# Kernel optimization log

Measured on AMD Instinct MI355X. Metric: run time of the kernel, lower is better.

## Reference

```python
import jax, jax.numpy as jnp
import numpy as np

N = 20000
E = 320000
IN_FEAT = 256
HID = 256
OUT_FEAT = 128


def setup_inputs() -> dict:
    key = jax.random.key(0)
    ks = jax.random.split(key, 10)
    inp = {
        "x": jax.random.normal(ks[0], (N, IN_FEAT), dtype=jnp.float32),
        "edge_src": jax.random.randint(ks[1], (E,), 0, N, dtype=jnp.int32),
        "edge_dst": jax.random.randint(ks[2], (E,), 0, N, dtype=jnp.int32),
        "edge_w": jax.random.uniform(ks[3], (E,), dtype=jnp.float32),
        # params (Linear weights stored as [out, in], torch convention)
        "W_emb": jax.random.normal(ks[4], (HID, IN_FEAT), dtype=jnp.float32) / np.sqrt(IN_FEAT),
        "W_gc1": jax.random.normal(ks[5], (HID, 2 * HID), dtype=jnp.float32) / np.sqrt(2 * HID),
        "b_gc1": jnp.zeros((HID,), dtype=jnp.float32),
        "W_gc2": jax.random.normal(ks[6], (HID, 2 * HID), dtype=jnp.float32) / np.sqrt(2 * HID),
        "b_gc2": jnp.zeros((HID,), dtype=jnp.float32),
        "W_fc": jax.random.normal(ks[7], (OUT_FEAT, HID), dtype=jnp.float32) / np.sqrt(HID),
    }
    return inp


def reference(x, edge_src, edge_dst, edge_w, W_emb, W_gc1, b_gc1, W_gc2, b_gc2, W_fc):
    n = x.shape[0]

    def adj_mul(h):
        msgs = h[edge_src] * edge_w[:, None]           # [E, hid]
        return jax.ops.segment_sum(msgs, edge_dst, num_segments=n)

    def gconv(h, W, b):
        cat = jnp.concatenate([h, adj_mul(h)], axis=1)  # [N, 2*hid]
        return cat @ W.T + b

    h = x @ W_emb.T                                    # embedding (no bias)
    h = h + jax.nn.relu(gconv(h, W_gc1, b_gc1))        # residual (dropout = eval identity)
    h = h + jax.nn.relu(gconv(h, W_gc2, b_gc2))
    out = h @ W_fc.T                                   # fc_last (no bias)
    out = out / jnp.sqrt(jnp.sum(out * out, axis=1, keepdims=True))
    return out
```

## Files before the change

kernel.cpp:

```cpp
#include <hip/hip_runtime.h>
#include <math.h>

#define N_NODES 20000
#define E_EDGES 320000
#define HID 256
#define OUT_FEAT 128
#define MPAD 20224
#define CAP 64

#define BM 128
#define BN 128
#define BK 64
#define LSTR 72

typedef __attribute__((ext_vector_type(8))) __bf16 bf16x8;
typedef __attribute__((ext_vector_type(4))) float floatx4;


#define WBLK 176
#define EBLK 1250

__global__ void convert_scatter_kernel(
    const float* __restrict__ w0, const float* __restrict__ w1,
    const float* __restrict__ w2, const float* __restrict__ w3,
    __bf16* __restrict__ o0, __bf16* __restrict__ o1,
    __bf16* __restrict__ o2, __bf16* __restrict__ o3,
    const int* __restrict__ src, const int* __restrict__ dst,
    const float* __restrict__ w, int* __restrict__ counts,
    int2* __restrict__ edges) {
    const int b = blockIdx.x;
    if (b < WBLK) {
        const size_t gi = ((size_t)b * 256 + threadIdx.x) * 8;
        const size_t s0 = 65536, s1 = s0 + 131072, s2 = s1 + 131072, s3 = s2 + 32768;
        if (gi >= s3) return;
        const float* srcp; __bf16* dstp; size_t off;
        if (gi < s0)      { srcp = w0; dstp = o0; off = gi; }
        else if (gi < s1) { srcp = w1; dstp = o1; off = gi - s0; }
        else if (gi < s2) { srcp = w2; dstp = o2; off = gi - s1; }
        else              { srcp = w3; dstp = o3; off = gi - s2; }
        float4 v0 = *(const float4*)(srcp + off);
        float4 v1 = *(const float4*)(srcp + off + 4);
        bf16x8 o;
        o[0] = (__bf16)v0.x; o[1] = (__bf16)v0.y; o[2] = (__bf16)v0.z; o[3] = (__bf16)v0.w;
        o[4] = (__bf16)v1.x; o[5] = (__bf16)v1.y; o[6] = (__bf16)v1.z; o[7] = (__bf16)v1.w;
        *(bf16x8*)(dstp + off) = o;
    } else {
        int e = (b - WBLK) * 256 + threadIdx.x;
        if (e < E_EDGES) {
            int d = dst[e];
            int p = atomicAdd(&counts[d], 1);
            edges[(size_t)d * CAP + p] = make_int2(src[e], __float_as_int(w[e]));
        }
    }
}


__global__ __launch_bounds__(256) void aggregate_kernel(
    const __bf16* __restrict__ h, const int* __restrict__ counts,
    const int2* __restrict__ edges, __bf16* __restrict__ agg) {
    const int w = threadIdx.x >> 6, lane = threadIdx.x & 63;
    const int half = lane >> 5, lh = lane & 31;
    const int d = blockIdx.x * 8 + w * 2 + half;
    const size_t base = (size_t)d * CAP;
    const int iters = (counts[d] + 15) >> 4;
    float acc[8];
#pragma unroll
    for (int q = 0; q < 8; q++) acc[q] = 0.f;

    for (int it = 0; it < iters; ++it) {
        const int2* ep = edges + base + it * 16;
        int4 eh[8];
#pragma unroll
        for (int u = 0; u < 8; u++) eh[u] = *(const int4*)(ep + u * 2);
        bf16x8 hv[16];
#pragma unroll
        for (int u = 0; u < 8; u++) {
            hv[u * 2]     = *(const bf16x8*)(h + (size_t)eh[u].x * HID + lh * 8);
            hv[u * 2 + 1] = *(const bf16x8*)(h + (size_t)eh[u].z * HID + lh * 8);
        }
#pragma unroll
        for (int u = 0; u < 8; u++) {
            float wa = __int_as_float(eh[u].y), wb = __int_as_float(eh[u].w);
#pragma unroll
            for (int q = 0; q < 8; q++) {
                acc[q] = fmaf(wa, (float)hv[u * 2][q], acc[q]);
                acc[q] = fmaf(wb, (float)hv[u * 2 + 1][q], acc[q]);
            }
        }
    }
    bf16x8 o;
#pragma unroll
    for (int q = 0; q < 8; q++) o[q] = (__bf16)acc[q];
    *(bf16x8*)(agg + (size_t)d * HID + lh * 8) = o;
}


template <int KTOT, int EPI, bool F32A>
__global__ __launch_bounds__(256) void gemm_tile_kernel(
    const __bf16* __restrict__ A1,
    const float* __restrict__ A1f,
    const __bf16* __restrict__ A2,
    const __bf16* __restrict__ W,
    const float* __restrict__ bias,
    const __bf16* __restrict__ hres,
    __bf16* __restrict__ outb)
{
    __shared__ __bf16 As[BM * LSTR];
    __shared__ __bf16 Bs[BN * LSTR];
    const int tid = threadIdx.x;
    const int row0 = blockIdx.y * BM;
    const int col0 = blockIdx.x * BN;
    const int wv = tid >> 6, l = tid & 63, lr = l & 15, lq = l >> 4;
    const int wm = wv & 1, wn = wv >> 1;

    floatx4 acc[4][4];
#pragma unroll
    for (int i = 0; i < 4; i++)
#pragma unroll
        for (int j = 0; j < 4; j++) acc[i][j] = (floatx4){0.f, 0.f, 0.f, 0.f};

    const int srow = tid >> 3;
    const int skq = (tid & 7) * 8;

    for (int kc = 0; kc < KTOT; kc += BK) {
        if (F32A) {
#pragma unroll
            for (int r = 0; r < 4; r++) {
                int row = r * 32 + srow;
                int grow = row0 + row;
                float4 v0 = make_float4(0.f, 0.f, 0.f, 0.f), v1 = v0;
                if (grow < N_NODES) {
                    const float* xp = A1f + (size_t)grow * HID + kc + skq;
                    v0 = *(const float4*)xp;
                    v1 = *(const float4*)(xp + 4);
                }
                bf16x8 o;
                o[0] = (__bf16)v0.x; o[1] = (__bf16)v0.y; o[2] = (__bf16)v0.z; o[3] = (__bf16)v0.w;
                o[4] = (__bf16)v1.x; o[5] = (__bf16)v1.y; o[6] = (__bf16)v1.z; o[7] = (__bf16)v1.w;
                *(bf16x8*)&As[row * LSTR + skq] = o;
            }
        } else {
            const __bf16* Asrc = (KTOT == 512 && kc >= 256) ? A2 : A1;
            const int ks = (KTOT == 512) ? (kc & 255) : kc;
#pragma unroll
            for (int r = 0; r < 4; r++) {
                int row = r * 32 + srow;
                *(bf16x8*)&As[row * LSTR + skq] =
                    *(const bf16x8*)(Asrc + (size_t)(row0 + row) * HID + ks + skq);
            }
        }
#pragma unroll
        for (int r = 0; r < 4; r++) {
            int row = r * 32 + srow;
            *(bf16x8*)&Bs[row * LSTR + skq] =
                *(const bf16x8*)(W + (size_t)(col0 + row) * KTOT + kc + skq);
        }
        __syncthreads();
#pragma unroll
        for (int s = 0; s < 2; s++) {
            bf16x8 af[4], bfr[4];
#pragma unroll
            for (int mt = 0; mt < 4; mt++)
                af[mt] = *(const bf16x8*)&As[(wm * 64 + mt * 16 + lr) * LSTR + s * 32 + lq * 8];
#pragma unroll
            for (int nt = 0; nt < 4; nt++)
                bfr[nt] = *(const bf16x8*)&Bs[(wn * 64 + nt * 16 + lr) * LSTR + s * 32 + lq * 8];
#pragma unroll
            for (int mt = 0; mt < 4; mt++)
#pragma unroll
                for (int nt = 0; nt < 4; nt++)
                    acc[mt][nt] = __builtin_amdgcn_mfma_f32_16x16x32_bf16(af[mt], bfr[nt], acc[mt][nt], 0, 0, 0);
        }
        __syncthreads();
    }

#pragma unroll
    for (int nt = 0; nt < 4; nt++) {
        const int col = col0 + wn * 64 + nt * 16 + lr;
        float b = 0.f;
        if (EPI == 1) b = bias[col];
#pragma unroll
        for (int mt = 0; mt < 4; mt++) {
            const int row = row0 + wm * 64 + mt * 16 + lq * 4;
#pragma unroll
            for (int r = 0; r < 4; r++) {
                float v = acc[mt][nt][r];
                if (EPI == 1) {
                    float res = (float)hres[(size_t)(row + r) * HID + col];
                    v = res + fmaxf(v + b, 0.f);
                }
                outb[(size_t)(row + r) * HID + col] = (__bf16)v;
            }
        }
    }
}


__global__ __launch_bounds__(256) void fc_norm_kernel(
    const __bf16* __restrict__ h,
    const __bf16* __restrict__ W,
    float* __restrict__ out)
{
    const int tid = threadIdx.x;
    const int wv = tid >> 6;
    const int l = tid & 63;
    const int lr = l & 15;
    const int lq = l >> 4;
    const int rowbase = blockIdx.x * 128 + wv * 32;

    floatx4 acc[2][8];
#pragma unroll
    for (int i = 0; i < 2; i++)
#pragma unroll
        for (int j = 0; j < 8; j++) acc[i][j] = (floatx4){0.f, 0.f, 0.f, 0.f};

#pragma unroll
    for (int kt = 0; kt < 256; kt += 32) {
        bf16x8 af[2], bfr[8];
#pragma unroll
        for (int mt = 0; mt < 2; mt++)
            af[mt] = *(const bf16x8*)(h + (size_t)(rowbase + mt * 16 + lr) * 256 + kt + lq * 8);
#pragma unroll
        for (int nt = 0; nt < 8; nt++)
            bfr[nt] = *(const bf16x8*)(W + (size_t)(nt * 16 + lr) * 256 + kt + lq * 8);
#pragma unroll
        for (int mt = 0; mt < 2; mt++)
#pragma unroll
            for (int nt = 0; nt < 8; nt++)
                acc[mt][nt] = __builtin_amdgcn_mfma_f32_16x16x32_bf16(af[mt], bfr[nt], acc[mt][nt], 0, 0, 0);
    }

#pragma unroll
    for (int mt = 0; mt < 2; mt++) {
        float s[4];
#pragma unroll
        for (int r = 0; r < 4; r++) {
            float t = 0.f;
#pragma unroll
            for (int nt = 0; nt < 8; nt++) t = fmaf(acc[mt][nt][r], acc[mt][nt][r], t);
            s[r] = t;
        }
#pragma unroll
        for (int mask = 1; mask <= 8; mask <<= 1) {
#pragma unroll
            for (int r = 0; r < 4; r++) s[r] += __shfl_xor(s[r], mask);
        }
        float inv[4];
#pragma unroll
        for (int r = 0; r < 4; r++) inv[r] = rsqrtf(s[r]);
#pragma unroll
        for (int r = 0; r < 4; r++) {
            int row = rowbase + mt * 16 + lq * 4 + r;
            if (row >= N_NODES) continue;
#pragma unroll
            for (int nt = 0; nt < 8; nt++)
                out[(size_t)row * OUT_FEAT + nt * 16 + lr] = acc[mt][nt][r] * inv[r];
        }
    }
}


extern "C" void kernel_launch(void* const* d_in, const int* in_sizes, int n_in,
                              void* d_out, int out_size, void* d_ws, size_t ws_size,
                              hipStream_t stream) {
    const float* x        = (const float*)d_in[0];
    const int*   edge_src = (const int*)d_in[1];
    const int*   edge_dst = (const int*)d_in[2];
    const float* edge_w   = (const float*)d_in[3];
    const float* W_emb    = (const float*)d_in[4];
    const float* W_gc1    = (const float*)d_in[5];
    const float* b_gc1    = (const float*)d_in[6];
    const float* W_gc2    = (const float*)d_in[7];
    const float* b_gc2    = (const float*)d_in[8];
    const float* W_fc     = (const float*)d_in[9];
    float* out = (float*)d_out;

    char* p = (char*)d_ws;
    const size_t HROW = (size_t)MPAD * HID;
    __bf16* hb0   = (__bf16*)p;             p += HROW * 2;
    __bf16* hb1   = (__bf16*)p;             p += HROW * 2;
    __bf16* aggb  = (__bf16*)p;             p += HROW * 2;
    __bf16* wemb  = (__bf16*)p;             p += 65536 * 2;
    __bf16* w1b   = (__bf16*)p;             p += 131072 * 2;
    __bf16* w2b   = (__bf16*)p;             p += 131072 * 2;
    __bf16* wfcb  = (__bf16*)p;             p += 32768 * 2;
    int2*   edges = (int2*)p;               p += (size_t)N_NODES * CAP * 8;
    int*    counts = (int*)p;               p += (size_t)MPAD * 4;

    hipMemsetAsync(counts, 0, (size_t)MPAD * 4, stream);
    hipMemsetAsync(edges, 0, (size_t)N_NODES * CAP * 8, stream);

    convert_scatter_kernel<<<WBLK + EBLK, 256, 0, stream>>>(
        W_emb, W_gc1, W_gc2, W_fc, wemb, w1b, w2b, wfcb,
        edge_src, edge_dst, edge_w, counts, edges);

    const dim3 grid_g(HID / BN, MPAD / BM);

    gemm_tile_kernel<256, 0, true><<<grid_g, 256, 0, stream>>>(
        nullptr, x, nullptr, wemb, nullptr, nullptr, hb0);
    aggregate_kernel<<<N_NODES / 8, 256, 0, stream>>>(hb0, counts, edges, aggb);
    gemm_tile_kernel<512, 1, false><<<grid_g, 256, 0, stream>>>(
        hb0, nullptr, aggb, w1b, b_gc1, hb0, hb1);
    aggregate_kernel<<<N_NODES / 8, 256, 0, stream>>>(hb1, counts, edges, aggb);
    gemm_tile_kernel<512, 1, false><<<grid_g, 256, 0, stream>>>(
        hb1, nullptr, aggb, w2b, b_gc2, hb1, hb0);
    fc_norm_kernel<<<MPAD / 128, 256, 0, stream>>>(hb0, wfcb, out);
}
```

Baseline: 208.5 us.

## Fuse second graph conv with final FC and row normalization; use 64-row GEMM tiles

Shrinks GEMM tiles from 128x128 to 64x128 so the grid has more blocks for the 20k-row problem. Replaces the last gconv GEMM plus the separate fc_norm kernel with one 512-thread kernel. That kernel computes a full 64x256 output tile, writes the residual+ReLU result into shared memory, then runs the FC and L2 normalization from LDS. This removes a global write and read of h and one launch, at the cost of redundant loads of W_gc2 per block and an FC phase that uses only half the waves.

```diff
diff --git a/kernel.cpp b/kernel.cpp
--- a/kernel.cpp
+++ b/kernel.cpp
@@ -8,8 +8,6 @@
 #define MPAD 20224
 #define CAP 64
 
-#define BM 128
-#define BN 128
 #define BK 64
 #define LSTR 72
 
@@ -96,7 +94,7 @@
 
 
 template <int KTOT, int EPI, bool F32A>
-__global__ __launch_bounds__(256) void gemm_tile_kernel(
+__global__ __launch_bounds__(256) void gemm64_kernel(
     const __bf16* __restrict__ A1,
     const float* __restrict__ A1f,
     const __bf16* __restrict__ A2,
@@ -105,17 +103,17 @@
     const __bf16* __restrict__ hres,
     __bf16* __restrict__ outb)
 {
-    __shared__ __bf16 As[BM * LSTR];
-    __shared__ __bf16 Bs[BN * LSTR];
+    __shared__ __bf16 As[64 * LSTR];
+    __shared__ __bf16 Bs[128 * LSTR];
     const int tid = threadIdx.x;
-    const int row0 = blockIdx.y * BM;
-    const int col0 = blockIdx.x * BN;
+    const int row0 = blockIdx.y * 64;
+    const int col0 = blockIdx.x * 128;
     const int wv = tid >> 6, l = tid & 63, lr = l & 15, lq = l >> 4;
     const int wm = wv & 1, wn = wv >> 1;
 
-    floatx4 acc[4][4];
-#pragma unroll
-    for (int i = 0; i < 4; i++)
+    floatx4 acc[2][4];
+#pragma unroll
+    for (int i = 0; i < 2; i++)
 #pragma unroll
         for (int j = 0; j < 4; j++) acc[i][j] = (floatx4){0.f, 0.f, 0.f, 0.f};
 
@@ -125,7 +123,7 @@
     for (int kc = 0; kc < KTOT; kc += BK) {
         if (F32A) {
 #pragma unroll
-            for (int r = 0; r < 4; r++) {
+            for (int r = 0; r < 2; r++) {
                 int row = r * 32 + srow;
                 int grow = row0 + row;
                 float4 v0 = make_float4(0.f, 0.f, 0.f, 0.f), v1 = v0;
@@ -143,7 +141,7 @@
             const __bf16* Asrc = (KTOT == 512 && kc >= 256) ? A2 : A1;
             const int ks = (KTOT == 512) ? (kc & 255) : kc;
 #pragma unroll
-            for (int r = 0; r < 4; r++) {
+            for (int r = 0; r < 2; r++) {
                 int row = r * 32 + srow;
                 *(bf16x8*)&As[row * LSTR + skq] =
                     *(const bf16x8*)(Asrc + (size_t)(row0 + row) * HID + ks + skq);
@@ -158,15 +156,15 @@
         __syncthreads();
 #pragma unroll
         for (int s = 0; s < 2; s++) {
-            bf16x8 af[4], bfr[4];
-#pragma unroll
-            for (int mt = 0; mt < 4; mt++)
-                af[mt] = *(const bf16x8*)&As[(wm * 64 + mt * 16 + lr) * LSTR + s * 32 + lq * 8];
+            bf16x8 af[2], bfr[4];
+#pragma unroll
+            for (int mt = 0; mt < 2; mt++)
+                af[mt] = *(const bf16x8*)&As[(wm * 32 + mt * 16 + lr) * LSTR + s * 32 + lq * 8];
 #pragma unroll
             for (int nt = 0; nt < 4; nt++)
                 bfr[nt] = *(const bf16x8*)&Bs[(wn * 64 + nt * 16 + lr) * LSTR + s * 32 + lq * 8];
 #pragma unroll
-            for (int mt = 0; mt < 4; mt++)
+            for (int mt = 0; mt < 2; mt++)
 #pragma unroll
                 for (int nt = 0; nt < 4; nt++)
                     acc[mt][nt] = __builtin_amdgcn_mfma_f32_16x16x32_bf16(af[mt], bfr[nt], acc[mt][nt], 0, 0, 0);
@@ -180,8 +178,8 @@
         float b = 0.f;
         if (EPI == 1) b = bias[col];
 #pragma unroll
-        for (int mt = 0; mt < 4; mt++) {
-            const int row = row0 + wm * 64 + mt * 16 + lq * 4;
+        for (int mt = 0; mt < 2; mt++) {
+            const int row = row0 + wm * 32 + mt * 16 + lq * 4;
 #pragma unroll
             for (int r = 0; r < 4; r++) {
                 float v = acc[mt][nt][r];
@@ -196,48 +194,102 @@
 }
 
 
-__global__ __launch_bounds__(256) void fc_norm_kernel(
-    const __bf16* __restrict__ h,
+#define TSTR 264
+
+__global__ __launch_bounds__(512) void gconv_fc_kernel(
+    const __bf16* __restrict__ hp,
+    const __bf16* __restrict__ ag,
     const __bf16* __restrict__ W,
-    float* __restrict__ out)
+    const float* __restrict__ bias,
+    const __bf16* __restrict__ Wfc,
+    float* __restrict__ outp)
 {
+    __shared__ __bf16 smem[64 * LSTR + 256 * LSTR];
+    __bf16* As = smem;
+    __bf16* Bs = smem + 64 * LSTR;
     const int tid = threadIdx.x;
-    const int wv = tid >> 6;
-    const int l = tid & 63;
-    const int lr = l & 15;
-    const int lq = l >> 4;
-    const int rowbase = blockIdx.x * 128 + wv * 32;
-
-    floatx4 acc[2][8];
+    const int row0 = blockIdx.x * 64;
+    const int wv = tid >> 6, l = tid & 63, lr = l & 15, lq = l >> 4;
+    const int wm = wv & 1, wn4 = wv >> 1;
+
+    floatx4 acc[2][4];
 #pragma unroll
     for (int i = 0; i < 2; i++)
 #pragma unroll
-        for (int j = 0; j < 8; j++) acc[i][j] = (floatx4){0.f, 0.f, 0.f, 0.f};
-
-#pragma unroll
-    for (int kt = 0; kt < 256; kt += 32) {
-        bf16x8 af[2], bfr[8];
-#pragma unroll
-        for (int mt = 0; mt < 2; mt++)
-            af[mt] = *(const bf16x8*)(h + (size_t)(rowbase + mt * 16 + lr) * 256 + kt + lq * 8);
-#pragma unroll
-        for (int nt = 0; nt < 8; nt++)
-            bfr[nt] = *(const bf16x8*)(W + (size_t)(nt * 16 + lr) * 256 + kt + lq * 8);
-#pragma unroll
-        for (int mt = 0; mt < 2; mt++)
+        for (int j = 0; j < 4; j++) acc[i][j] = (floatx4){0.f, 0.f, 0.f, 0.f};
+
+    const int srow = tid >> 3;
+    const int skq = (tid & 7) * 8;
+
+    for (int kc = 0; kc < 512; kc += BK) {
+        const __bf16* Asrc = (kc >= 256) ? ag : hp;
+        const int ks = kc & 255;
+        *(bf16x8*)&As[srow * LSTR + skq] =
+            *(const bf16x8*)(Asrc + (size_t)(row0 + srow) * HID + ks + skq);
+#pragma unroll
+        for (int r = 0; r < 4; r++) {
+            int row = r * 64 + srow;
+            *(bf16x8*)&Bs[row * LSTR + skq] =
+                *(const bf16x8*)(W + (size_t)row * 512 + kc + skq);
+        }
+        __syncthreads();
+#pragma unroll
+        for (int s = 0; s < 2; s++) {
+            bf16x8 af[2], bfr[4];
+#pragma unroll
+            for (int mt = 0; mt < 2; mt++)
+                af[mt] = *(const bf16x8*)&As[(wm * 32 + mt * 16 + lr) * LSTR + s * 32 + lq * 8];
+#pragma unroll
+            for (int nt = 0; nt < 4; nt++)
+                bfr[nt] = *(const bf16x8*)&Bs[(wn4 * 64 + nt * 16 + lr) * LSTR + s * 32 + lq * 8];
+#pragma unroll
+            for (int mt = 0; mt < 2; mt++)
+#pragma unroll
+                for (int nt = 0; nt < 4; nt++)
+                    acc[mt][nt] = __builtin_amdgcn_mfma_f32_16x16x32_bf16(af[mt], bfr[nt], acc[mt][nt], 0, 0, 0);
+        }
+        __syncthreads();
+    }
+
+    __bf16 (*tile)[TSTR] = (__bf16(*)[TSTR])smem;
+#pragma unroll
+    for (int nt = 0; nt < 4; nt++) {
+        const int col = wn4 * 64 + nt * 16 + lr;
+        const float b = bias[col];
+#pragma unroll
+        for (int mt = 0; mt < 2; mt++) {
+            const int lrow = wm * 32 + mt * 16 + lq * 4;
+#pragma unroll
+            for (int r = 0; r < 4; r++) {
+                float res = (float)hp[(size_t)(row0 + lrow + r) * HID + col];
+                float v = res + fmaxf(acc[mt][nt][r] + b, 0.f);
+                tile[lrow + r][col] = (__bf16)v;
+            }
+        }
+    }
+    __syncthreads();
+
+    if (wv < 4) {
+        floatx4 facc[8];
+#pragma unroll
+        for (int j = 0; j < 8; j++) facc[j] = (floatx4){0.f, 0.f, 0.f, 0.f};
+#pragma unroll
+        for (int kt = 0; kt < 256; kt += 32) {
+            bf16x8 a = *(const bf16x8*)&tile[wv * 16 + lr][kt + lq * 8];
+            bf16x8 bf8[8];
 #pragma unroll
             for (int nt = 0; nt < 8; nt++)
-                acc[mt][nt] = __builtin_amdgcn_mfma_f32_16x16x32_bf16(af[mt], bfr[nt], acc[mt][nt], 0, 0, 0);
-    }
-
-#pragma unroll
-    for (int mt = 0; mt < 2; mt++) {
+                bf8[nt] = *(const bf16x8*)(Wfc + (size_t)(nt * 16 + lr) * 256 + kt + lq * 8);
+#pragma unroll
+            for (int nt = 0; nt < 8; nt++)
+                facc[nt] = __builtin_amdgcn_mfma_f32_16x16x32_bf16(a, bf8[nt], facc[nt], 0, 0, 0);
+        }
         float s[4];
 #pragma unroll
         for (int r = 0; r < 4; r++) {
             float t = 0.f;
 #pragma unroll
-            for (int nt = 0; nt < 8; nt++) t = fmaf(acc[mt][nt][r], acc[mt][nt][r], t);
+            for (int nt = 0; nt < 8; nt++) t = fmaf(facc[nt][r], facc[nt][r], t);
             s[r] = t;
         }
 #pragma unroll
@@ -250,11 +302,11 @@
         for (int r = 0; r < 4; r++) inv[r] = rsqrtf(s[r]);
 #pragma unroll
         for (int r = 0; r < 4; r++) {
-            int row = rowbase + mt * 16 + lq * 4 + r;
+            int row = row0 + wv * 16 + lq * 4 + r;
             if (row >= N_NODES) continue;
 #pragma unroll
             for (int nt = 0; nt < 8; nt++)
-                out[(size_t)row * OUT_FEAT + nt * 16 + lr] = acc[mt][nt][r] * inv[r];
+                outp[(size_t)row * OUT_FEAT + nt * 16 + lr] = facc[nt][r] * inv[r];
         }
     }
 }
@@ -294,15 +346,13 @@
         W_emb, W_gc1, W_gc2, W_fc, wemb, w1b, w2b, wfcb,
         edge_src, edge_dst, edge_w, counts, edges);
 
-    const dim3 grid_g(HID / BN, MPAD / BM);
-
-    gemm_tile_kernel<256, 0, true><<<grid_g, 256, 0, stream>>>(
+    const dim3 grid_g(2, MPAD / 64);
+
+    gemm64_kernel<256, 0, true><<<grid_g, 256, 0, stream>>>(
         nullptr, x, nullptr, wemb, nullptr, nullptr, hb0);
     aggregate_kernel<<<N_NODES / 8, 256, 0, stream>>>(hb0, counts, edges, aggb);
-    gemm_tile_kernel<512, 1, false><<<grid_g, 256, 0, stream>>>(
+    gemm64_kernel<512, 1, false><<<grid_g, 256, 0, stream>>>(
         hb0, nullptr, aggb, w1b, b_gc1, hb0, hb1);
     aggregate_kernel<<<N_NODES / 8, 256, 0, stream>>>(hb1, counts, edges, aggb);
-    gemm_tile_kernel<512, 1, false><<<grid_g, 256, 0, stream>>>(
-        hb1, nullptr, aggb, w2b, b_gc2, hb1, hb0);
-    fc_norm_kernel<<<MPAD / 128, 256, 0, stream>>>(hb0, wfcb, out);
-}
+    gconv_fc_kernel<<<MPAD / 64, 512, 0, stream>>>(hb1, aggb, w2b, b_gc2, wfcb, out);
+}
```

New measurement: 203.6 us. -2.4%, faster.
